# Performance work log

Measured on AMD Instinct MI355X. Metric: run time of the kernel, lower is better.

## Reference

```python
import jax, jax.numpy as jnp
import numpy as np


def setup_inputs() -> dict:
    key = jax.random.key(0)
    ks = jax.random.split(key, 7)
    B, T, C, H = 4, 4096, 1024, 64
    x = jax.random.normal(ks[0], (B, T, C), dtype=jnp.float32)
    Wq = jax.random.normal(ks[1], (C, H), dtype=jnp.float32) * 0.02
    bq = jax.random.normal(ks[2], (H,), dtype=jnp.float32) * 0.02
    Wk = jax.random.normal(ks[3], (C, H), dtype=jnp.float32) * 0.02
    bk = jax.random.normal(ks[4], (H,), dtype=jnp.float32) * 0.02
    Wv = jax.random.normal(ks[5], (C, H), dtype=jnp.float32) * 0.02
    bv = jax.random.normal(ks[6], (H,), dtype=jnp.float32) * 0.02
    return {"x": x, "Wq": Wq, "bq": bq, "Wk": Wk, "bk": bk, "Wv": Wv, "bv": bv}


def reference(x, Wq, bq, Wk, bk, Wv, bv):
    B, T, C = x.shape
    q = x @ Wq + bq            # [B,T,H]
    k = x @ Wk + bk            # [B,T,H]
    v = x @ Wv + bv            # [B,T,H]
    # NOTE: original scales by C**-0.5 where C = n_embd (input dim), not head_size
    scale = jnp.asarray(C, x.dtype) ** -0.5
    wei = jnp.einsum('bth,bsh->bts', q, k) * scale   # [B,T,T]
    causal = jnp.tril(jnp.ones((T, T), dtype=bool))
    wei = jnp.where(causal, wei, -jnp.inf)
    wei = jax.nn.softmax(wei, axis=-1)
    out = jnp.einsum('bts,bsh->bth', wei, v)         # [B,T,H]
    return out
```

## Files before the change

### kernel.cpp

```cpp
#include <hip/hip_runtime.h>
#include <hip/hip_bf16.h>

#define T_DIM 4096
#define C_DIM 1024
#define H_DIM 64
#define B_DIM 4

typedef __attribute__((ext_vector_type(8))) short short8v;
typedef __attribute__((ext_vector_type(4))) short short4v;
typedef __attribute__((ext_vector_type(4))) float float4v;

__device__ __forceinline__ unsigned short f2bf(float f) {
    __hip_bfloat16 h = __float2bfloat16(f);
    return *reinterpret_cast<unsigned short*>(&h);
}
__device__ __forceinline__ float bf2f(unsigned short u) {
    __hip_bfloat16 h = *reinterpret_cast<__hip_bfloat16*>(&u);
    return __bfloat162float(h);
}

__device__ __forceinline__ int vperm(int t5) {
    return ((t5 & 12) << 1) | (t5 & 3) | ((t5 & 16) >> 2);
}

#define GLL16(gsrc, ldst)                                                         \
    __builtin_amdgcn_global_load_lds(                                             \
        (const __attribute__((address_space(1))) unsigned int*)(gsrc),            \
        (__attribute__((address_space(3))) unsigned int*)(ldst), 16, 0, 0)

__global__ __launch_bounds__(256) void wprep(
    const float* __restrict__ Wq, const float* __restrict__ Wk,
    const float* __restrict__ Wv, unsigned short* __restrict__ wt)
{
    const int tid = blockIdx.x * 256 + threadIdx.x;
    const int k   = tid & 1023;
    const int col = (tid >> 10) & 63;
    const int m   = tid >> 16;
    const float* __restrict__ W = (m == 0) ? Wq : (m == 1) ? Wk : Wv;
    wt[tid] = f2bf(W[k * 64 + col]);
}

__global__ __launch_bounds__(512, 2) void qkv_gemm(
    const float* __restrict__ x, const unsigned short* __restrict__ wt,
    const float* __restrict__ bq, const float* __restrict__ bk,
    const float* __restrict__ bv,
    unsigned short* __restrict__ qb, unsigned short* __restrict__ kmat,
    unsigned short* __restrict__ vP)
{
    __shared__ __align__(16) unsigned char lx[2][16384];
    __shared__ __align__(16) unsigned char lw[2][24576];

    const int t    = threadIdx.x;
    const int w    = t >> 6;
    const int lane = t & 63;
    const int l15  = lane & 15;
    const int g    = lane >> 4;
    const int r0   = blockIdx.x * 64;

    const int xgl = (t & 15) ^ ((t >> 4) & 15);
    const int wgl = (t & 7) ^ ((t >> 3) & 7);

    const unsigned char* __restrict__ xB = (const unsigned char*)x;
    const unsigned char* __restrict__ wB = (const unsigned char*)wt;

#define STAGE(p, kb)                                                              \
    {                                                                             \
        _Pragma("unroll")                                                         \
        for (int i = 0; i < 2; ++i) {                                             \
            const unsigned char* src =                                            \
                xB + (size_t)(r0 + i * 32 + (t >> 4)) * 4096 + (kb) * 256 + xgl * 16; \
            GLL16(src, &lx[p][(i * 512 + t) * 16]);                               \
        }                                                                         \
        _Pragma("unroll")                                                         \
        for (int j = 0; j < 3; ++j) {                                             \
            const unsigned char* src =                                            \
                wB + (size_t)(j * 64 + (t >> 3)) * 2048 + (kb) * 128 + wgl * 16;  \
            GLL16(src, &lw[p][(j * 512 + t) * 16]);                               \
        }                                                                         \
    }

    const int rbase = (w & 3) * 16;
    const int W0    = (w >> 2) * 96;

    float4v acc[6];
#pragma unroll
    for (int cg = 0; cg < 6; ++cg) acc[cg] = (float4v){0.f, 0.f, 0.f, 0.f};

    STAGE(0, 0);
    __syncthreads();

    for (int kb = 0; kb < 16; ++kb) {
        const int p = kb & 1;
        if (kb < 15) STAGE(p ^ 1, kb + 1);

        const int arow = rbase + l15;
        short8v af[2];
#pragma unroll
        for (int ks = 0; ks < 2; ++ks) {
            const int Lg0 = ks * 8 + 2 * g;
            const float4 a0 = *(const float4*)&lx[p][arow * 256 + ((Lg0)     ^ l15) * 16];
            const float4 a1 = *(const float4*)&lx[p][arow * 256 + ((Lg0 + 1) ^ l15) * 16];
            short8v a;
            a[0] = (short)f2bf(a0.x); a[1] = (short)f2bf(a0.y);
            a[2] = (short)f2bf(a0.z); a[3] = (short)f2bf(a0.w);
            a[4] = (short)f2bf(a1.x); a[5] = (short)f2bf(a1.y);
            a[6] = (short)f2bf(a1.z); a[7] = (short)f2bf(a1.w);
            af[ks] = a;
        }

#pragma unroll
        for (int cg = 0; cg < 6; ++cg) {
            const int wrow = W0 + cg * 16 + l15;
#pragma unroll
            for (int ks = 0; ks < 2; ++ks) {
                const int phys = (ks * 4 + g) ^ (l15 & 7);
                const short8v bf = *(const short8v*)&lw[p][wrow * 128 + phys * 16];
                acc[cg] = __builtin_amdgcn_mfma_f32_16x16x32_bf16(af[ks], bf, acc[cg], 0, 0, 0);
            }
        }
        __syncthreads();
    }

    const float qs = 0.03125f * 1.44269504088896f;
#pragma unroll
    for (int cg = 0; cg < 6; ++cg) {
        const int cabs = W0 + cg * 16 + l15;
        const int m    = cabs >> 6;
        const int h    = cabs & 63;
        const float bb = ((m == 0) ? bq : (m == 1) ? bk : bv)[h];
#pragma unroll
        for (int rr = 0; rr < 4; ++rr) {
            const int row = r0 + rbase + 4 * g + rr;
            const float vv = acc[cg][rr] + bb;
            if (m == 0) {
                qb[(size_t)row * 64 + h] = f2bf(vv * qs);
            } else if (m == 1) {
                kmat[(size_t)row * 64 + h] = f2bf(vv);
            } else {
                const int b_i = row >> 12;
                const int tt  = row & 4095;
                const int tp  = (tt & ~31) | vperm(tt & 31);
                vP[((size_t)b_i * 64 + h) * T_DIM + tp] = f2bf(vv);
            }
        }
    }
#undef STAGE
}

__global__ __launch_bounds__(512, 4) void attn_mfma(
    const unsigned short* __restrict__ qb, const unsigned short* __restrict__ kmat,
    const unsigned short* __restrict__ vP, float* __restrict__ out)
{
    __shared__ float partO[8][32][68];
    __shared__ float partl[8][32];

    const int w    = threadIdx.x >> 6;
    const int lane = threadIdx.x & 63;
    const int l15  = lane & 15;
    const int g    = lane >> 4;
    const int i    = blockIdx.x;
    const int p2   = (i & 255) >> 2;
    const int b    = i & 3;
    const int tt   = (i < 256) ? (127 - p2) : p2;
    const int q0   = tt * 32;
    const int n    = tt + 1;

    const unsigned short* __restrict__ qbase = qb + ((size_t)b * T_DIM + q0) * 64;
    short8v qf[2][2];
    qf[0][0] = *(const short8v*)(qbase + (size_t)l15 * 64 + 8 * g);
    qf[0][1] = *(const short8v*)(qbase + (size_t)l15 * 64 + 32 + 8 * g);
    qf[1][0] = *(const short8v*)(qbase + (size_t)(16 + l15) * 64 + 8 * g);
    qf[1][1] = *(const short8v*)(qbase + (size_t)(16 + l15) * 64 + 32 + 8 * g);

    const unsigned short* __restrict__ kbase = kmat + (size_t)b * T_DIM * 64;
    const unsigned short* __restrict__ vbase = vP + (size_t)b * 64 * T_DIM;

    float4v acc[2][4];
#pragma unroll
    for (int qt = 0; qt < 2; ++qt)
#pragma unroll
        for (int f = 0; f < 4; ++f) acc[qt][f] = (float4v){0.f, 0.f, 0.f, 0.f};
    float lsum[2] = {0.f, 0.f};

    const int rem = n & 7;
    const int cnt = (n >> 3) + (w < rem ? 1 : 0);
    const int st  = w * (n >> 3) + (w < rem ? w : rem);

    for (int s = 0; s < cnt; ++s) {
        const int kv0 = (st + s) * 32;

        const unsigned short* kr0 = kbase + (size_t)(kv0 + l15) * 64 + 8 * g;
        const unsigned short* kr1 = kr0 + 16 * 64;
        const short8v ka0 = *(const short8v*)kr0;
        const short8v ka1 = *(const short8v*)(kr0 + 32);
        const short8v ka2 = *(const short8v*)kr1;
        const short8v ka3 = *(const short8v*)(kr1 + 32);

        short8v vb4[4];
#pragma unroll
        for (int f = 0; f < 4; ++f)
            vb4[f] = *(const short8v*)(
                vbase + (size_t)(f * 16 + l15) * T_DIM + kv0 + 8 * g);

#pragma unroll
        for (int qt = 0; qt < 2; ++qt) {
            const float4v z = (float4v){0.f, 0.f, 0.f, 0.f};
            float4v slo = __builtin_amdgcn_mfma_f32_16x16x32_bf16(ka0, qf[qt][0], z, 0, 0, 0);
            slo = __builtin_amdgcn_mfma_f32_16x16x32_bf16(ka1, qf[qt][1], slo, 0, 0, 0);
            float4v shi = __builtin_amdgcn_mfma_f32_16x16x32_bf16(ka2, qf[qt][0], z, 0, 0, 0);
            shi = __builtin_amdgcn_mfma_f32_16x16x32_bf16(ka3, qf[qt][1], shi, 0, 0, 0);

            const int qabs = q0 + 16 * qt + l15;
            short8v pa;
            float ls = 0.f;
#pragma unroll
            for (int r = 0; r < 4; ++r) {
                const int kvlo = kv0 + 4 * g + r;
                const float plo = (kvlo <= qabs) ? exp2f(slo[r]) : 0.f;
                const float phi = (kvlo + 16 <= qabs) ? exp2f(shi[r]) : 0.f;
                const unsigned short ulo = f2bf(plo);
                const unsigned short uhi = f2bf(phi);
                pa[r]     = (short)ulo;
                pa[4 + r] = (short)uhi;
                ls += bf2f(ulo) + bf2f(uhi);
            }
            lsum[qt] += ls;
#pragma unroll
            for (int f = 0; f < 4; ++f)
                acc[qt][f] = __builtin_amdgcn_mfma_f32_16x16x32_bf16(pa, vb4[f], acc[qt][f], 0, 0, 0);
        }
    }

#pragma unroll
    for (int qt = 0; qt < 2; ++qt) {
        lsum[qt] += __shfl_xor(lsum[qt], 16);
        lsum[qt] += __shfl_xor(lsum[qt], 32);
    }

#pragma unroll
    for (int qt = 0; qt < 2; ++qt)
#pragma unroll
        for (int f = 0; f < 4; ++f)
#pragma unroll
            for (int r = 0; r < 4; ++r)
                partO[w][16 * qt + 4 * g + r][16 * f + l15] = acc[qt][f][r];
    if (g == 0) {
        partl[w][l15]      = lsum[0];
        partl[w][16 + l15] = lsum[1];
    }
    __syncthreads();

    const int row = threadIdx.x >> 4;
    const int c0  = (threadIdx.x & 15) * 4;
    float lt = 0.f;
#pragma unroll
    for (int ww = 0; ww < 8; ++ww) lt += partl[ww][row];
    const float inv = 1.f / lt;
    float4 o = make_float4(0.f, 0.f, 0.f, 0.f);
#pragma unroll
    for (int ww = 0; ww < 8; ++ww) {
        const float4 s = *(const float4*)&partO[ww][row][c0];
        o.x += s.x; o.y += s.y; o.z += s.z; o.w += s.w;
    }
    o.x *= inv; o.y *= inv; o.z *= inv; o.w *= inv;
    *(float4*)(out + ((size_t)b * T_DIM + q0 + row) * 64 + c0) = o;
}

extern "C" void kernel_launch(void* const* d_in, const int* in_sizes, int n_in,
                              void* d_out, int out_size, void* d_ws, size_t ws_size,
                              hipStream_t stream) {
    const float* x  = (const float*)d_in[0];
    const float* Wq = (const float*)d_in[1];
    const float* bq = (const float*)d_in[2];
    const float* Wk = (const float*)d_in[3];
    const float* bk = (const float*)d_in[4];
    const float* Wv = (const float*)d_in[5];
    const float* bv = (const float*)d_in[6];
    float* out = (float*)d_out;

    const size_t rows = (size_t)B_DIM * T_DIM;
    char* ws = (char*)d_ws;
    unsigned short* qb   = (unsigned short*)ws;
    unsigned short* kmat = qb + rows * H_DIM;
    unsigned short* vP   = kmat + rows * H_DIM;
    unsigned short* wt   = vP + rows * H_DIM;

    wprep<<<768, 256, 0, stream>>>(Wq, Wk, Wv, wt);
    qkv_gemm<<<256, 512, 0, stream>>>(x, wt, bq, bk, bv, qb, kmat, vP);
    attn_mfma<<<512, 512, 0, stream>>>(qb, kmat, vP, out);
}
```

Baseline: 65.97 us.

## Restructure QKV GEMM with split-K waves, smaller row tiles, and tiled weight transpose

The weight-prep kernel now transposes through a shared-memory tile with vectorized loads and stores instead of doing strided scalar reads. The QKV GEMM uses 32-row blocks, which doubles the grid to 512. Inside each block the K dimension is split across two wave groups whose partial sums are reduced through LDS. x is converted to bf16 once when it is staged into LDS, replacing the per-wave conversion on every read. In attention, tiles that lie fully below the diagonal skip the causal masking. The row sum now uses the unrounded fp32 probabilities instead of their bf16-rounded values, which shifts normalization slightly.

```diff
diff --git a/kernel.cpp b/kernel.cpp
--- a/kernel.cpp
+++ b/kernel.cpp
@@ -14,10 +14,6 @@
     __hip_bfloat16 h = __float2bfloat16(f);
     return *reinterpret_cast<unsigned short*>(&h);
 }
-__device__ __forceinline__ float bf2f(unsigned short u) {
-    __hip_bfloat16 h = *reinterpret_cast<__hip_bfloat16*>(&u);
-    return __bfloat162float(h);
-}
 
 __device__ __forceinline__ int vperm(int t5) {
     return ((t5 & 12) << 1) | (t5 & 3) | ((t5 & 16) >> 2);
@@ -32,12 +28,31 @@
     const float* __restrict__ Wq, const float* __restrict__ Wk,
     const float* __restrict__ Wv, unsigned short* __restrict__ wt)
 {
-    const int tid = blockIdx.x * 256 + threadIdx.x;
-    const int k   = tid & 1023;
-    const int col = (tid >> 10) & 63;
-    const int m   = tid >> 16;
+    __shared__ float tile[64][65];
+    const int t  = threadIdx.x;
+    const int m  = blockIdx.x >> 4;
+    const int k0 = (blockIdx.x & 15) * 64;
     const float* __restrict__ W = (m == 0) ? Wq : (m == 1) ? Wk : Wv;
-    wt[tid] = f2bf(W[k * 64 + col]);
+
+    const int kr = t >> 4, c4 = (t & 15) * 4;
+#pragma unroll
+    for (int j = 0; j < 4; ++j) {
+        const int row = kr + j * 16;
+        const float4 v = *(const float4*)(W + (size_t)(k0 + row) * 64 + c4);
+        tile[row][c4 + 0] = v.x; tile[row][c4 + 1] = v.y;
+        tile[row][c4 + 2] = v.z; tile[row][c4 + 3] = v.w;
+    }
+    __syncthreads();
+
+    const int col = t >> 2, q = t & 3;
+    short8v s0, s1;
+#pragma unroll
+    for (int j = 0; j < 8; ++j) s0[j] = (short)f2bf(tile[q * 16 + j][col]);
+#pragma unroll
+    for (int j = 0; j < 8; ++j) s1[j] = (short)f2bf(tile[q * 16 + 8 + j][col]);
+    unsigned short* dst = wt + (size_t)(m * 64 + col) * 1024 + k0 + q * 16;
+    *(short8v*)dst = s0;
+    *(short8v*)(dst + 8) = s1;
 }
 
 __global__ __launch_bounds__(512, 2) void qkv_gemm(
@@ -47,104 +62,128 @@
     unsigned short* __restrict__ qb, unsigned short* __restrict__ kmat,
     unsigned short* __restrict__ vP)
 {
-    __shared__ __align__(16) unsigned char lx[2][16384];
+    __shared__ __align__(16) unsigned char lx[2][4096];
     __shared__ __align__(16) unsigned char lw[2][24576];
 
     const int t    = threadIdx.x;
+    const int lane = t & 63;
     const int w    = t >> 6;
-    const int lane = t & 63;
     const int l15  = lane & 15;
-    const int g    = lane >> 4;
-    const int r0   = blockIdx.x * 64;
-
-    const int xgl = (t & 15) ^ ((t >> 4) & 15);
-    const int wgl = (t & 7) ^ ((t >> 3) & 7);
-
-    const unsigned char* __restrict__ xB = (const unsigned char*)x;
+    const int g4   = lane >> 4;
+    const int r0   = blockIdx.x * 32;
+
+    const int rg  = w & 1;
+    const int cgr = (w >> 1) & 1;
+    const int kh  = w >> 2;
+
+    const int srow  = t >> 3;
+    const int soct  = t & 7;
+    const int sphys = soct ^ (srow & 7);
+    const float* __restrict__ xsrc = x + (size_t)(r0 + srow) * C_DIM + soct * 8;
+    const int wgs = (t & 7) ^ ((t >> 3) & 7);
     const unsigned char* __restrict__ wB = (const unsigned char*)wt;
 
-#define STAGE(p, kb)                                                              \
+    float4v acc[6];
+#pragma unroll
+    for (int cg = 0; cg < 6; ++cg) acc[cg] = (float4v){0.f, 0.f, 0.f, 0.f};
+
+#define WSTAGE(p, kb)                                                             \
     {                                                                             \
         _Pragma("unroll")                                                         \
-        for (int i = 0; i < 2; ++i) {                                             \
-            const unsigned char* src =                                            \
-                xB + (size_t)(r0 + i * 32 + (t >> 4)) * 4096 + (kb) * 256 + xgl * 16; \
-            GLL16(src, &lx[p][(i * 512 + t) * 16]);                               \
-        }                                                                         \
-        _Pragma("unroll")                                                         \
-        for (int j = 0; j < 3; ++j) {                                             \
-            const unsigned char* src =                                            \
-                wB + (size_t)(j * 64 + (t >> 3)) * 2048 + (kb) * 128 + wgl * 16;  \
-            GLL16(src, &lw[p][(j * 512 + t) * 16]);                               \
-        }                                                                         \
-    }
-
-    const int rbase = (w & 3) * 16;
-    const int W0    = (w >> 2) * 96;
-
-    float4v acc[6];
-#pragma unroll
-    for (int cg = 0; cg < 6; ++cg) acc[cg] = (float4v){0.f, 0.f, 0.f, 0.f};
-
-    STAGE(0, 0);
+        for (int i = 0; i < 3; ++i)                                               \
+            GLL16(wB + (size_t)(i * 64 + (t >> 3)) * 2048 + (kb) * 128 + wgs * 16,\
+                  &lw[p][(i * 512 + t) * 16]);                                    \
+    }
+
+    WSTAGE(0, 0);
+    if (t < 256) {
+        const float4 a0 = *(const float4*)(xsrc);
+        const float4 a1 = *(const float4*)(xsrc + 4);
+        short8v xs;
+        xs[0] = (short)f2bf(a0.x); xs[1] = (short)f2bf(a0.y);
+        xs[2] = (short)f2bf(a0.z); xs[3] = (short)f2bf(a0.w);
+        xs[4] = (short)f2bf(a1.x); xs[5] = (short)f2bf(a1.y);
+        xs[6] = (short)f2bf(a1.z); xs[7] = (short)f2bf(a1.w);
+        *(short8v*)&lx[0][srow * 128 + sphys * 16] = xs;
+    }
     __syncthreads();
+
+    const int arow = rg * 16 + l15;
+    const int axor = arow & 7;
+    const int kg   = kh * 4 + g4;
 
     for (int kb = 0; kb < 16; ++kb) {
         const int p = kb & 1;
-        if (kb < 15) STAGE(p ^ 1, kb + 1);
-
-        const int arow = rbase + l15;
-        short8v af[2];
-#pragma unroll
-        for (int ks = 0; ks < 2; ++ks) {
-            const int Lg0 = ks * 8 + 2 * g;
-            const float4 a0 = *(const float4*)&lx[p][arow * 256 + ((Lg0)     ^ l15) * 16];
-            const float4 a1 = *(const float4*)&lx[p][arow * 256 + ((Lg0 + 1) ^ l15) * 16];
-            short8v a;
-            a[0] = (short)f2bf(a0.x); a[1] = (short)f2bf(a0.y);
-            a[2] = (short)f2bf(a0.z); a[3] = (short)f2bf(a0.w);
-            a[4] = (short)f2bf(a1.x); a[5] = (short)f2bf(a1.y);
-            a[6] = (short)f2bf(a1.z); a[7] = (short)f2bf(a1.w);
-            af[ks] = a;
-        }
-
+        float4 na = {0,0,0,0}, nb = {0,0,0,0};
+        if (kb < 15) {
+            if (t < 256) {
+                na = *(const float4*)(xsrc + (kb + 1) * 64);
+                nb = *(const float4*)(xsrc + (kb + 1) * 64 + 4);
+            }
+            WSTAGE(p ^ 1, kb + 1);
+        }
+
+        const short8v af = *(const short8v*)&lx[p][arow * 128 + (kg ^ axor) * 16];
 #pragma unroll
         for (int cg = 0; cg < 6; ++cg) {
-            const int wrow = W0 + cg * 16 + l15;
-#pragma unroll
-            for (int ks = 0; ks < 2; ++ks) {
-                const int phys = (ks * 4 + g) ^ (l15 & 7);
-                const short8v bf = *(const short8v*)&lw[p][wrow * 128 + phys * 16];
-                acc[cg] = __builtin_amdgcn_mfma_f32_16x16x32_bf16(af[ks], bf, acc[cg], 0, 0, 0);
+            const int col = cgr * 96 + cg * 16 + l15;
+            const short8v bf =
+                *(const short8v*)&lw[p][col * 128 + ((kg ^ (col & 7))) * 16];
+            acc[cg] = __builtin_amdgcn_mfma_f32_16x16x32_bf16(af, bf, acc[cg], 0, 0, 0);
+        }
+
+        if (kb < 15 && t < 256) {
+            short8v xs;
+            xs[0] = (short)f2bf(na.x); xs[1] = (short)f2bf(na.y);
+            xs[2] = (short)f2bf(na.z); xs[3] = (short)f2bf(na.w);
+            xs[4] = (short)f2bf(nb.x); xs[5] = (short)f2bf(nb.y);
+            xs[6] = (short)f2bf(nb.z); xs[7] = (short)f2bf(nb.w);
+            *(short8v*)&lx[p ^ 1][srow * 128 + sphys * 16] = xs;
+        }
+        __syncthreads();
+    }
+
+    float* comm = (float*)lw;
+    if (kh == 1) {
+        const int base = ((w - 4) * 64 + lane) * 24;
+#pragma unroll
+        for (int cg = 0; cg < 6; ++cg)
+#pragma unroll
+            for (int e = 0; e < 4; ++e) comm[base + cg * 4 + e] = acc[cg][e];
+    }
+    __syncthreads();
+    if (kh == 0) {
+        const int base = (w * 64 + lane) * 24;
+#pragma unroll
+        for (int cg = 0; cg < 6; ++cg)
+#pragma unroll
+            for (int e = 0; e < 4; ++e) acc[cg][e] += comm[base + cg * 4 + e];
+
+        const float qs = 0.03125f * 1.44269504088896f;
+#pragma unroll
+        for (int cg = 0; cg < 6; ++cg) {
+            const int cabs = cgr * 96 + cg * 16 + l15;
+            const int m    = cabs >> 6;
+            const int h    = cabs & 63;
+            const float bb = ((m == 0) ? bq : (m == 1) ? bk : bv)[h];
+#pragma unroll
+            for (int rr = 0; rr < 4; ++rr) {
+                const int row = r0 + rg * 16 + 4 * g4 + rr;
+                const float vv = acc[cg][rr] + bb;
+                if (m == 0) {
+                    qb[(size_t)row * 64 + h] = f2bf(vv * qs);
+                } else if (m == 1) {
+                    kmat[(size_t)row * 64 + h] = f2bf(vv);
+                } else {
+                    const int b_i = row >> 12;
+                    const int tt  = row & 4095;
+                    const int tp  = (tt & ~31) | vperm(tt & 31);
+                    vP[((size_t)b_i * 64 + h) * T_DIM + tp] = f2bf(vv);
+                }
             }
         }
-        __syncthreads();
-    }
-
-    const float qs = 0.03125f * 1.44269504088896f;
-#pragma unroll
-    for (int cg = 0; cg < 6; ++cg) {
-        const int cabs = W0 + cg * 16 + l15;
-        const int m    = cabs >> 6;
-        const int h    = cabs & 63;
-        const float bb = ((m == 0) ? bq : (m == 1) ? bk : bv)[h];
-#pragma unroll
-        for (int rr = 0; rr < 4; ++rr) {
-            const int row = r0 + rbase + 4 * g + rr;
-            const float vv = acc[cg][rr] + bb;
-            if (m == 0) {
-                qb[(size_t)row * 64 + h] = f2bf(vv * qs);
-            } else if (m == 1) {
-                kmat[(size_t)row * 64 + h] = f2bf(vv);
-            } else {
-                const int b_i = row >> 12;
-                const int tt  = row & 4095;
-                const int tp  = (tt & ~31) | vperm(tt & 31);
-                vP[((size_t)b_i * 64 + h) * T_DIM + tp] = f2bf(vv);
-            }
-        }
-    }
-#undef STAGE
+    }
+#undef WSTAGE
 }
 
 __global__ __launch_bounds__(512, 4) void attn_mfma(
@@ -210,19 +249,28 @@
             float4v shi = __builtin_amdgcn_mfma_f32_16x16x32_bf16(ka2, qf[qt][0], z, 0, 0, 0);
             shi = __builtin_amdgcn_mfma_f32_16x16x32_bf16(ka3, qf[qt][1], shi, 0, 0, 0);
 
-            const int qabs = q0 + 16 * qt + l15;
             short8v pa;
             float ls = 0.f;
-#pragma unroll
-            for (int r = 0; r < 4; ++r) {
-                const int kvlo = kv0 + 4 * g + r;
-                const float plo = (kvlo <= qabs) ? exp2f(slo[r]) : 0.f;
-                const float phi = (kvlo + 16 <= qabs) ? exp2f(shi[r]) : 0.f;
-                const unsigned short ulo = f2bf(plo);
-                const unsigned short uhi = f2bf(phi);
-                pa[r]     = (short)ulo;
-                pa[4 + r] = (short)uhi;
-                ls += bf2f(ulo) + bf2f(uhi);
+            if (kv0 + 31 <= q0 + 16 * qt) {
+#pragma unroll
+                for (int r = 0; r < 4; ++r) {
+                    const float plo = exp2f(slo[r]);
+                    const float phi = exp2f(shi[r]);
+                    pa[r]     = (short)f2bf(plo);
+                    pa[4 + r] = (short)f2bf(phi);
+                    ls += plo + phi;
+                }
+            } else {
+                const int qabs = q0 + 16 * qt + l15;
+#pragma unroll
+                for (int r = 0; r < 4; ++r) {
+                    const int kvlo = kv0 + 4 * g + r;
+                    const float plo = (kvlo <= qabs) ? exp2f(slo[r]) : 0.f;
+                    const float phi = (kvlo + 16 <= qabs) ? exp2f(shi[r]) : 0.f;
+                    pa[r]     = (short)f2bf(plo);
+                    pa[4 + r] = (short)f2bf(phi);
+                    ls += plo + phi;
+                }
             }
             lsum[qt] += ls;
 #pragma unroll
@@ -285,7 +333,7 @@
     unsigned short* vP   = kmat + rows * H_DIM;
     unsigned short* wt   = vP + rows * H_DIM;
 
-    wprep<<<768, 256, 0, stream>>>(Wq, Wk, Wv, wt);
-    qkv_gemm<<<256, 512, 0, stream>>>(x, wt, bq, bk, bv, qb, kmat, vP);
+    wprep<<<48, 256, 0, stream>>>(Wq, Wk, Wv, wt);
+    qkv_gemm<<<512, 512, 0, stream>>>(x, wt, bq, bk, bv, qb, kmat, vP);
     attn_mfma<<<512, 512, 0, stream>>>(qb, kmat, vP, out);
 }
```

Result: faster. 63.02 us (-4.5%).
